# Performance work log

Hardware: AMD Instinct MI355X
Metric: run time of the kernel (lower is better)

The kernel has to match this reference:

```python
import jax, jax.numpy as jnp
import numpy as np

HIDDEN = 1024
HEADS = 16
HEAD = HIDDEN // HEADS  # 64, rotary_emb_dim == head dim
B = 8
S = 1024  # max_seqlen; all sequences full length
WINDOW = (64, 64)  # sliding_window=128 -> (64, 64)
ROPE_BASE = 10000.0


def _rope_cos_sin(seqlen, dim, base):
    inv_freq = 1.0 / (base ** (jnp.arange(0, dim, 2, dtype=jnp.float32) / dim))
    t = jnp.arange(seqlen, dtype=jnp.float32)
    freqs = jnp.outer(t, inv_freq)  # [S, dim/2]
    return jnp.cos(freqs), jnp.sin(freqs)


def _apply_rope(x, cos, sin):
    # x: [B, S, H, D], non-interleaved rotary over full head dim
    d2 = cos.shape[-1]
    x1, x2 = x[..., :d2], x[..., d2:]
    c = cos[None, :, None, :]
    s = sin[None, :, None, :]
    return jnp.concatenate([x1 * c - x2 * s, x2 * c + x1 * s], axis=-1)


def setup_inputs() -> dict:
    key = jax.random.key(0)
    k1, k2, k3 = jax.random.split(key, 3)
    hidden_states = jax.random.normal(k1, (B * S, HIDDEN), dtype=jnp.float32)
    cu_seqlens = jnp.arange(B + 1, dtype=jnp.int32) * S
    indices = jnp.arange(B * S, dtype=jnp.int32)
    attn_mask = jnp.ones((B, S), dtype=jnp.int32)
    Wqkv = jax.random.normal(k2, (3 * HIDDEN, HIDDEN), dtype=jnp.float32) * 0.02
    Wo = jax.random.normal(k3, (HIDDEN, HIDDEN), dtype=jnp.float32) * 0.02
    return {
        'hidden_states': hidden_states,
        'cu_seqlens': cu_seqlens,
        'max_seqlen': S,
        'indices': indices,
        'attn_mask': attn_mask,
        'Wqkv': Wqkv,
        'Wo': Wo,
    }


def reference(hidden_states, cu_seqlens, max_seqlen, indices, attn_mask, Wqkv, Wo):
    # QKV projection on unpadded tokens: [T, 3*H*D]
    qkv = hidden_states @ Wqkv.T
    qkv = qkv.reshape(B, S, 3, HEADS, HEAD)
    # Rotary positions reset per sequence; all sequences are full length S.
    cos, sin = _rope_cos_sin(S, HEAD, ROPE_BASE)
    q = _apply_rope(qkv[:, :, 0], cos, sin)
    k = _apply_rope(qkv[:, :, 1], cos, sin)
    v = qkv[:, :, 2]
    scores = jnp.einsum('bshd,bthd->bhst', q, k) / jnp.sqrt(jnp.float32(HEAD))
    # sliding-window mask: key j visible to query i iff i-left <= j <= i+right
    i = jnp.arange(S)[:, None]
    j = jnp.arange(S)[None, :]
    win = (j >= i - WINDOW[0]) & (j <= i + WINDOW[1])  # [S, S]
    key_mask = attn_mask.astype(bool)[:, None, None, :]  # [B,1,1,S]
    mask = win[None, None, :, :] & key_mask
    scores = jnp.where(mask, scores, jnp.finfo(scores.dtype).min)
    probs = jax.nn.softmax(scores, axis=-1)
    attn = jnp.einsum('bhst,bthd->bshd', probs, v).reshape(B * S, HIDDEN)
    return attn @ Wo.T
```

## Files before the change

### kernel.cpp

```cpp
#include <hip/hip_runtime.h>


typedef __attribute__((ext_vector_type(8))) short short8;
typedef __attribute__((ext_vector_type(4))) float f32x4;

#define SEQ   1024
#define NHEAD 16
#define HEADD 64
#define NTOK  8192

__device__ __forceinline__ unsigned short f2bf(float x) {
  unsigned u = __float_as_uint(x);
  u += 0x7fffu + ((u >> 16) & 1u);
  return (unsigned short)(u >> 16);
}

__device__ __forceinline__ void gload_lds16(const void* g, void* l) {
  __builtin_amdgcn_global_load_lds((__attribute__((address_space(1))) void*)(g),
                                   (__attribute__((address_space(3))) void*)(l),
                                   16, 0, 0);
}

__global__ __launch_bounds__(256) void prep(
    const float* __restrict__ hidden, const float* __restrict__ Wqkv,
    const float* __restrict__ Wo,
    unsigned short* __restrict__ hb, unsigned short* __restrict__ wqb,
    unsigned short* __restrict__ wob, float2* __restrict__ tab) {
  int bid = blockIdx.x;
  const float* in; unsigned short* out; int i;
  if (bid < 8192)       { in = hidden; out = hb;  i = bid * 256 + threadIdx.x; }
  else if (bid < 11264) { in = Wqkv;   out = wqb; i = (bid - 8192) * 256 + threadIdx.x; }
  else if (bid < 12288) { in = Wo;     out = wob; i = (bid - 11264) * 256 + threadIdx.x; }
  else {
    int j = (bid - 12288) * 256 + threadIdx.x;
    int s = j >> 5, d = j & 31;
    float inv = exp2f(-(float)d * 0.41524101186092034f);
    float sn, cs;
    sincosf((float)s * inv, &sn, &cs);
    tab[j] = make_float2(cs, sn);
    return;
  }
  float4 v = ((const float4*)in)[i];
  ushort4 o;
  o.x = f2bf(v.x); o.y = f2bf(v.y); o.z = f2bf(v.z); o.w = f2bf(v.w);
  ((ushort4*)out)[i] = o;
}

__global__ __launch_bounds__(256) void gemm_qkv_rope(
    const unsigned short* __restrict__ A,
    const unsigned short* __restrict__ W,
    const float2* __restrict__ tab,
    unsigned short* __restrict__ qb,
    unsigned short* __restrict__ kb,
    unsigned short* __restrict__ vt)
{
  __shared__ unsigned short As[128 * 32];
  __shared__ unsigned short Bs[128 * 32];
  const int tid  = threadIdx.x;
  const int wave = tid >> 6, lane = tid & 63;
  const int quad = lane >> 4, l15 = lane & 15;
  const int bid  = blockIdx.x;
  const int xcd  = bid & 7, idx = bid >> 3;
  const int rb   = xcd * 8 + (idx & 7);
  const int cb   = idx >> 3;
  const int row0 = rb * 128;
  const int col0 = cb * 128;
  const int mrow = (wave >> 1) * 64;
  const int ncol = (wave & 1) * 64;
  const int qs8  = (quad ^ ((l15 >> 1) & 3)) * 8;

  f32x4 acc[4][4];
#pragma unroll
  for (int i = 0; i < 4; i++)
#pragma unroll
    for (int j = 0; j < 4; j++) acc[i][j] = (f32x4){0.f, 0.f, 0.f, 0.f};

  for (int k0 = 0; k0 < 1024; k0 += 32) {
#pragma unroll
    for (int i = 0; i < 2; i++) {
      int p = i * 256 + tid;
      int r = p >> 2, c = p & 3;
      int cs = c ^ ((r >> 1) & 3);
      gload_lds16(A + (size_t)(row0 + r) * 1024 + k0 + cs * 8, &As[p * 8]);
      gload_lds16(W + (size_t)(col0 + r) * 1024 + k0 + cs * 8, &Bs[p * 8]);
    }
    __syncthreads();
    short8 af[4], bf[4];
#pragma unroll
    for (int mt = 0; mt < 4; mt++)
      af[mt] = *(const short8*)&As[(mrow + mt * 16 + l15) * 32 + qs8];
#pragma unroll
    for (int nt = 0; nt < 4; nt++)
      bf[nt] = *(const short8*)&Bs[(ncol + nt * 16 + l15) * 32 + qs8];
#pragma unroll
    for (int mt = 0; mt < 4; mt++)
#pragma unroll
      for (int nt = 0; nt < 4; nt++)
        acc[mt][nt] = __builtin_amdgcn_mfma_f32_16x16x32_bf16(af[mt], bf[nt],
                                                              acc[mt][nt], 0, 0, 0);
    __syncthreads();
  }

  const int colw  = col0 + ncol;
  const int which = colw >> 10;
  const int h     = (colw >> 6) & 15;
  const int rowg  = row0 + mrow;

  if (which == 2) {
#pragma unroll
    for (int mt = 0; mt < 4; mt++) {
      int rbase = rowg + mt * 16 + quad * 4;
      int b = rbase >> 10, s = rbase & 1023;
#pragma unroll
      for (int c = 0; c < 4; c++) {
        int d = c * 16 + l15;
        ushort4 o;
        o.x = f2bf(acc[mt][c][0]); o.y = f2bf(acc[mt][c][1]);
        o.z = f2bf(acc[mt][c][2]); o.w = f2bf(acc[mt][c][3]);
        *(ushort4*)&vt[((size_t)((b * 16 + h) * 64 + d)) * 1024 + s] = o;
      }
    }
  } else {
    unsigned short* dst = (which == 0) ? qb : kb;
    const float scale = (which == 0) ? 0.125f : 1.0f;
#pragma unroll
    for (int mt = 0; mt < 4; mt++) {
#pragma unroll
      for (int r = 0; r < 4; r++) {
        int row = rowg + mt * 16 + quad * 4 + r;
        int b = row >> 10, s = row & 1023;
        size_t base = (size_t)((b * 16 + h) * 1024 + s) * 64;
        float2 t0 = tab[s * 32 + l15];
        float2 t1 = tab[s * 32 + 16 + l15];
        float x1a = acc[mt][0][r], x2a = acc[mt][2][r];
        float x1b = acc[mt][1][r], x2b = acc[mt][3][r];
        dst[base + l15]           = f2bf((x1a * t0.x - x2a * t0.y) * scale);
        dst[base + 32 + l15]      = f2bf((x2a * t0.x + x1a * t0.y) * scale);
        dst[base + 16 + l15]      = f2bf((x1b * t1.x - x2b * t1.y) * scale);
        dst[base + 48 + l15]      = f2bf((x2b * t1.x + x1b * t1.y) * scale);
      }
    }
  }
}

__global__ __launch_bounds__(256) void attn_win(
    const unsigned short* __restrict__ qb,
    const unsigned short* __restrict__ kb,
    const unsigned short* __restrict__ vt,
    const int* __restrict__ am,
    unsigned short* __restrict__ ob)
{
  __shared__ unsigned short Ks[192 * 68];
  __shared__ unsigned short Vs[64 * 196];
  __shared__ unsigned short smask[192];

  const int tid  = threadIdx.x;
  const int wave = tid >> 6, lane = tid & 63;
  const int quad = lane >> 4, l15 = lane & 15;
  const int b  = blockIdx.x >> 4, h = blockIdx.x & 15;
  const int qs = blockIdx.y * 64;
  const size_t hb = (size_t)(b * 16 + h);
  const unsigned short* Qg = qb + hb * SEQ * 64;
  const unsigned short* Kg = kb + hb * SEQ * 64;
  const unsigned short* Vg = vt + hb * 64 * SEQ;
  const int t0 = qs - 64;

#pragma unroll
  for (int i = 0; i < 6; i++) {
    int p = i * 256 + tid;
    int r = p >> 3, c = p & 7;
    int t = t0 + r; t = t < 0 ? 0 : (t > 1023 ? 1023 : t);
    *(short8*)&Ks[r * 68 + c * 8] = *(const short8*)&Kg[(size_t)t * 64 + c * 8];
  }
#pragma unroll
  for (int i = 0; i < 6; i++) {
    int p = i * 256 + tid;
    int d = p / 24, c = p % 24;
    int t = t0 + c * 8; t = t < 0 ? 0 : (t > 1016 ? 1016 : t);
    *(short8*)&Vs[d * 196 + c * 8] = *(const short8*)&Vg[(size_t)d * SEQ + t];
  }
  if (tid < 192) {
    int t = t0 + tid;
    smask[tid] = (t >= 0 && t < SEQ) ? (unsigned short)(am[b * SEQ + t] != 0) : 0;
  }
  __syncthreads();

  const int qw = qs + wave * 16;
  short8 qf0 = *(const short8*)&Qg[(size_t)(qw + l15) * 64 + quad * 8];
  short8 qf1 = *(const short8*)&Qg[(size_t)(qw + l15) * 64 + 32 + quad * 8];

  f32x4 sc[12];
#pragma unroll
  for (int tt = 0; tt < 12; tt++) {
    short8 b0 = *(const short8*)&Ks[(tt * 16 + l15) * 68 + quad * 8];
    short8 b1 = *(const short8*)&Ks[(tt * 16 + l15) * 68 + 32 + quad * 8];
    f32x4 a = (f32x4){0.f, 0.f, 0.f, 0.f};
    a = __builtin_amdgcn_mfma_f32_16x16x32_bf16(qf0, b0, a, 0, 0, 0);
    a = __builtin_amdgcn_mfma_f32_16x16x32_bf16(qf1, b1, a, 0, 0, 0);
    sc[tt] = a;
  }

  float lrow[4];
#pragma unroll
  for (int r = 0; r < 4; r++) {
    int i = qw + quad * 4 + r;
    float mx = -3e38f;
#pragma unroll
    for (int tt = 0; tt < 12; tt++) {
      int t = t0 + tt * 16 + l15;
      bool ok = (t >= i - 64) && (t <= i + 64) && smask[tt * 16 + l15];
      float v = ok ? sc[tt][r] : -3e38f;
      sc[tt][r] = v;
      mx = fmaxf(mx, v);
    }
#pragma unroll
    for (int off = 1; off < 16; off <<= 1) mx = fmaxf(mx, __shfl_xor(mx, off));
    float sum = 0.f;
#pragma unroll
    for (int tt = 0; tt < 12; tt++) {
      float p = __expf(sc[tt][r] - mx);
      sc[tt][r] = p;
      sum += p;
    }
#pragma unroll
    for (int off = 1; off < 16; off <<= 1) sum += __shfl_xor(sum, off);
    lrow[r] = sum;
  }

  __syncthreads();
  unsigned short* Pw = &Ks[wave * (16 * 196)];
#pragma unroll
  for (int tt = 0; tt < 12; tt++)
#pragma unroll
    for (int r = 0; r < 4; r++)
      Pw[(quad * 4 + r) * 196 + tt * 16 + l15] = f2bf(sc[tt][r]);
  __syncthreads();

  f32x4 o[4];
#pragma unroll
  for (int dt = 0; dt < 4; dt++) o[dt] = (f32x4){0.f, 0.f, 0.f, 0.f};
#pragma unroll
  for (int kt = 0; kt < 6; kt++) {
    short8 pf = *(const short8*)&Pw[l15 * 196 + kt * 32 + quad * 8];
#pragma unroll
    for (int dt = 0; dt < 4; dt++) {
      short8 vf = *(const short8*)&Vs[(dt * 16 + l15) * 196 + kt * 32 + quad * 8];
      o[dt] = __builtin_amdgcn_mfma_f32_16x16x32_bf16(pf, vf, o[dt], 0, 0, 0);
    }
  }

#pragma unroll
  for (int r = 0; r < 4; r++) {
    float inv = 1.f / lrow[r];
    int tok = b * SEQ + qw + quad * 4 + r;
    size_t base = (size_t)tok * 1024 + h * 64;
#pragma unroll
    for (int dt = 0; dt < 4; dt++)
      ob[base + dt * 16 + l15] = f2bf(o[dt][r] * inv);
  }
}

__global__ __launch_bounds__(256) void gemm_out(
    const unsigned short* __restrict__ A,
    const unsigned short* __restrict__ W,
    float* __restrict__ out)
{
  __shared__ unsigned short As[128 * 32];
  __shared__ unsigned short Bs[128 * 32];
  const int tid  = threadIdx.x;
  const int wave = tid >> 6, lane = tid & 63;
  const int quad = lane >> 4, l15 = lane & 15;
  const int bid  = blockIdx.x;
  const int xcd  = bid & 7, idx = bid >> 3;
  const int row0 = (xcd * 8 + (idx & 7)) * 128;
  const int col0 = (idx >> 3) * 128;
  const int mrow = (wave >> 1) * 64;
  const int ncol = (wave & 1) * 64;
  const int qs8  = (quad ^ ((l15 >> 1) & 3)) * 8;

  f32x4 acc[4][4];
#pragma unroll
  for (int i = 0; i < 4; i++)
#pragma unroll
    for (int j = 0; j < 4; j++) acc[i][j] = (f32x4){0.f, 0.f, 0.f, 0.f};

  for (int k0 = 0; k0 < 1024; k0 += 32) {
#pragma unroll
    for (int i = 0; i < 2; i++) {
      int p = i * 256 + tid;
      int r = p >> 2, c = p & 3;
      int cs = c ^ ((r >> 1) & 3);
      gload_lds16(A + (size_t)(row0 + r) * 1024 + k0 + cs * 8, &As[p * 8]);
      gload_lds16(W + (size_t)(col0 + r) * 1024 + k0 + cs * 8, &Bs[p * 8]);
    }
    __syncthreads();
    short8 af[4], bf[4];
#pragma unroll
    for (int mt = 0; mt < 4; mt++)
      af[mt] = *(const short8*)&As[(mrow + mt * 16 + l15) * 32 + qs8];
#pragma unroll
    for (int nt = 0; nt < 4; nt++)
      bf[nt] = *(const short8*)&Bs[(ncol + nt * 16 + l15) * 32 + qs8];
#pragma unroll
    for (int mt = 0; mt < 4; mt++)
#pragma unroll
      for (int nt = 0; nt < 4; nt++)
        acc[mt][nt] = __builtin_amdgcn_mfma_f32_16x16x32_bf16(af[mt], bf[nt],
                                                              acc[mt][nt], 0, 0, 0);
    __syncthreads();
  }

  const int colw = col0 + ncol;
  const int rowg = row0 + mrow;
#pragma unroll
  for (int mt = 0; mt < 4; mt++)
#pragma unroll
    for (int r = 0; r < 4; r++) {
      int row = rowg + mt * 16 + quad * 4 + r;
#pragma unroll
      for (int nt = 0; nt < 4; nt++)
        out[(size_t)row * 1024 + colw + nt * 16 + l15] = acc[mt][nt][r];
    }
}

extern "C" void kernel_launch(void* const* d_in, const int* in_sizes, int n_in,
                              void* d_out, int out_size, void* d_ws, size_t ws_size,
                              hipStream_t stream) {
  const float* hidden = (const float*)d_in[0];
  const int*   am     = (const int*)d_in[4];
  const float* Wqkv   = (const float*)d_in[5];
  const float* Wo     = (const float*)d_in[6];
  float* out = (float*)d_out;

  char* ws = (char*)d_ws;
  unsigned short* hb  = (unsigned short*)(ws);
  unsigned short* wqb = (unsigned short*)(ws + (size_t)(16 << 20));
  unsigned short* wob = (unsigned short*)(ws + (size_t)(22 << 20));
  unsigned short* qbf = (unsigned short*)(ws + (size_t)(24 << 20));
  unsigned short* kbf = (unsigned short*)(ws + (size_t)(40 << 20));
  unsigned short* vtb = (unsigned short*)(ws + (size_t)(56 << 20));
  float2*         tab = (float2*)(ws + (size_t)(72 << 20));
  unsigned short* ab  = hb;

  prep<<<12416, 256, 0, stream>>>(hidden, Wqkv, Wo, hb, wqb, wob, tab);

  gemm_qkv_rope<<<1536, 256, 0, stream>>>(hb, wqb, tab, qbf, kbf, vtb);

  dim3 g2(128, 16);
  attn_win<<<g2, 256, 0, stream>>>(qbf, kbf, vtb, am, ab);

  gemm_out<<<512, 256, 0, stream>>>(ab, wob, out);
}
```

Baseline: 234.2 us.

## Fuse windowed attention and output GEMM into persistent kernel with grid barrier

New measurement: 311.9 us. 33.2% more time.

```diff
diff --git a/kernel.cpp b/kernel.cpp
--- a/kernel.cpp
+++ b/kernel.cpp
@@ -8,6 +8,7 @@
 #define NHEAD 16
 #define HEADD 64
 #define NTOK  8192
+#define FBLK  512
 
 __device__ __forceinline__ unsigned short f2bf(float x) {
   unsigned u = __float_as_uint(x);
@@ -19,6 +20,10 @@
   __builtin_amdgcn_global_load_lds((__attribute__((address_space(1))) void*)(g),
                                    (__attribute__((address_space(3))) void*)(l),
                                    16, 0, 0);
+}
+
+__global__ void binit(unsigned* bar) {
+  if (threadIdx.x < 2) bar[threadIdx.x] = 0u;
 }
 
 __global__ __launch_bounds__(256) void prep(
@@ -143,184 +148,201 @@
   }
 }
 
-__global__ __launch_bounds__(256) void attn_win(
+__global__ __launch_bounds__(256, 2) void attn_gemm2(
     const unsigned short* __restrict__ qb,
     const unsigned short* __restrict__ kb,
     const unsigned short* __restrict__ vt,
     const int* __restrict__ am,
-    unsigned short* __restrict__ ob)
+    unsigned short* __restrict__ ab,
+    const unsigned short* __restrict__ W,
+    float* __restrict__ out,
+    unsigned* __restrict__ bar)
 {
-  __shared__ unsigned short Ks[192 * 68];
-  __shared__ unsigned short Vs[64 * 196];
-  __shared__ unsigned short smask[192];
+  __shared__ union {
+    struct { unsigned short Ks[192 * 68];
+             unsigned short Vs[64 * 196];
+             unsigned short smask[192]; } a;
+    struct { unsigned short As[128 * 32];
+             unsigned short Bs[128 * 32]; } g;
+  } sm;
 
   const int tid  = threadIdx.x;
   const int wave = tid >> 6, lane = tid & 63;
   const int quad = lane >> 4, l15 = lane & 15;
-  const int b  = blockIdx.x >> 4, h = blockIdx.x & 15;
-  const int qs = blockIdx.y * 64;
+  const int bid  = blockIdx.x;
+
+  const int x = bid & 127;
+  const int b = x >> 4, h = x & 15;
   const size_t hb = (size_t)(b * 16 + h);
   const unsigned short* Qg = qb + hb * SEQ * 64;
   const unsigned short* Kg = kb + hb * SEQ * 64;
   const unsigned short* Vg = vt + hb * 64 * SEQ;
-  const int t0 = qs - 64;
-
-#pragma unroll
-  for (int i = 0; i < 6; i++) {
-    int p = i * 256 + tid;
-    int r = p >> 3, c = p & 7;
-    int t = t0 + r; t = t < 0 ? 0 : (t > 1023 ? 1023 : t);
-    *(short8*)&Ks[r * 68 + c * 8] = *(const short8*)&Kg[(size_t)t * 64 + c * 8];
-  }
-#pragma unroll
-  for (int i = 0; i < 6; i++) {
-    int p = i * 256 + tid;
-    int d = p / 24, c = p % 24;
-    int t = t0 + c * 8; t = t < 0 ? 0 : (t > 1016 ? 1016 : t);
-    *(short8*)&Vs[d * 196 + c * 8] = *(const short8*)&Vg[(size_t)d * SEQ + t];
-  }
-  if (tid < 192) {
-    int t = t0 + tid;
-    smask[tid] = (t >= 0 && t < SEQ) ? (unsigned short)(am[b * SEQ + t] != 0) : 0;
-  }
+
+  for (int it = 0; it < 4; it++) {
+    const int qt = ((bid >> 7) + 4 * it) & 15;
+    const int qs = qt * 64;
+    const int t0 = qs - 64;
+    __syncthreads();
+
+#pragma unroll
+    for (int i = 0; i < 6; i++) {
+      int p = i * 256 + tid;
+      int r = p >> 3, c = p & 7;
+      int t = t0 + r; t = t < 0 ? 0 : (t > 1023 ? 1023 : t);
+      *(short8*)&sm.a.Ks[r * 68 + c * 8] =
+          *(const short8*)&Kg[(size_t)t * 64 + c * 8];
+    }
+#pragma unroll
+    for (int i = 0; i < 6; i++) {
+      int p = i * 256 + tid;
+      int d = p / 24, c = p % 24;
+      int t = t0 + c * 8; t = t < 0 ? 0 : (t > 1016 ? 1016 : t);
+      *(short8*)&sm.a.Vs[d * 196 + c * 8] =
+          *(const short8*)&Vg[(size_t)d * SEQ + t];
+    }
+    if (tid < 192) {
+      int t = t0 + tid;
+      sm.a.smask[tid] = (t >= 0 && t < SEQ)
+                          ? (unsigned short)(am[b * SEQ + t] != 0) : 0;
+    }
+    __syncthreads();
+
+    const int qw = qs + wave * 16;
+    short8 qf0 = *(const short8*)&Qg[(size_t)(qw + l15) * 64 + quad * 8];
+    short8 qf1 = *(const short8*)&Qg[(size_t)(qw + l15) * 64 + 32 + quad * 8];
+
+    f32x4 sc[12];
+#pragma unroll
+    for (int tt = 0; tt < 12; tt++) {
+      short8 b0 = *(const short8*)&sm.a.Ks[(tt * 16 + l15) * 68 + quad * 8];
+      short8 b1 = *(const short8*)&sm.a.Ks[(tt * 16 + l15) * 68 + 32 + quad * 8];
+      f32x4 a = (f32x4){0.f, 0.f, 0.f, 0.f};
+      a = __builtin_amdgcn_mfma_f32_16x16x32_bf16(qf0, b0, a, 0, 0, 0);
+      a = __builtin_amdgcn_mfma_f32_16x16x32_bf16(qf1, b1, a, 0, 0, 0);
+      sc[tt] = a;
+    }
+
+    float lrow[4];
+#pragma unroll
+    for (int r = 0; r < 4; r++) {
+      int i = qw + quad * 4 + r;
+      float sum = 0.f;
+#pragma unroll
+      for (int tt = 0; tt < 12; tt++) {
+        int t = t0 + tt * 16 + l15;
+        bool ok = (t >= i - 64) && (t <= i + 64) && sm.a.smask[tt * 16 + l15];
+        float p = ok ? __expf(sc[tt][r]) : 0.f;
+        sc[tt][r] = p;
+        sum += p;
+      }
+#pragma unroll
+      for (int off = 1; off < 16; off <<= 1) sum += __shfl_xor(sum, off);
+      lrow[r] = sum;
+    }
+
+    __syncthreads();
+    unsigned short* Pw = &sm.a.Ks[wave * (16 * 196)];
+#pragma unroll
+    for (int tt = 0; tt < 12; tt++)
+#pragma unroll
+      for (int r = 0; r < 4; r++)
+        Pw[(quad * 4 + r) * 196 + tt * 16 + l15] = f2bf(sc[tt][r]);
+    __syncthreads();
+
+    f32x4 o[4];
+#pragma unroll
+    for (int dt = 0; dt < 4; dt++) o[dt] = (f32x4){0.f, 0.f, 0.f, 0.f};
+#pragma unroll
+    for (int kt = 0; kt < 6; kt++) {
+      short8 pf = *(const short8*)&Pw[l15 * 196 + kt * 32 + quad * 8];
+#pragma unroll
+      for (int dt = 0; dt < 4; dt++) {
+        short8 vf = *(const short8*)&sm.a.Vs[(dt * 16 + l15) * 196 +
+                                             kt * 32 + quad * 8];
+        o[dt] = __builtin_amdgcn_mfma_f32_16x16x32_bf16(pf, vf, o[dt], 0, 0, 0);
+      }
+    }
+
+#pragma unroll
+    for (int r = 0; r < 4; r++) {
+      float inv = 1.f / lrow[r];
+      int tok = b * SEQ + qw + quad * 4 + r;
+      size_t base = (size_t)tok * 1024 + h * 64;
+#pragma unroll
+      for (int dt = 0; dt < 4; dt++)
+        ab[base + dt * 16 + l15] = f2bf(o[dt][r] * inv);
+    }
+  }
+
   __syncthreads();
-
-  const int qw = qs + wave * 16;
-  short8 qf0 = *(const short8*)&Qg[(size_t)(qw + l15) * 64 + quad * 8];
-  short8 qf1 = *(const short8*)&Qg[(size_t)(qw + l15) * 64 + 32 + quad * 8];
-
-  f32x4 sc[12];
-#pragma unroll
-  for (int tt = 0; tt < 12; tt++) {
-    short8 b0 = *(const short8*)&Ks[(tt * 16 + l15) * 68 + quad * 8];
-    short8 b1 = *(const short8*)&Ks[(tt * 16 + l15) * 68 + 32 + quad * 8];
-    f32x4 a = (f32x4){0.f, 0.f, 0.f, 0.f};
-    a = __builtin_amdgcn_mfma_f32_16x16x32_bf16(qf0, b0, a, 0, 0, 0);
-    a = __builtin_amdgcn_mfma_f32_16x16x32_bf16(qf1, b1, a, 0, 0, 0);
-    sc[tt] = a;
-  }
-
-  float lrow[4];
-#pragma unroll
-  for (int r = 0; r < 4; r++) {
-    int i = qw + quad * 4 + r;
-    float mx = -3e38f;
-#pragma unroll
-    for (int tt = 0; tt < 12; tt++) {
-      int t = t0 + tt * 16 + l15;
-      bool ok = (t >= i - 64) && (t <= i + 64) && smask[tt * 16 + l15];
-      float v = ok ? sc[tt][r] : -3e38f;
-      sc[tt][r] = v;
-      mx = fmaxf(mx, v);
-    }
-#pragma unroll
-    for (int off = 1; off < 16; off <<= 1) mx = fmaxf(mx, __shfl_xor(mx, off));
-    float sum = 0.f;
-#pragma unroll
-    for (int tt = 0; tt < 12; tt++) {
-      float p = __expf(sc[tt][r] - mx);
-      sc[tt][r] = p;
-      sum += p;
-    }
-#pragma unroll
-    for (int off = 1; off < 16; off <<= 1) sum += __shfl_xor(sum, off);
-    lrow[r] = sum;
-  }
-
+  if (tid == 0) {
+    __threadfence();
+    unsigned a = atomicAdd(&bar[0], 1u);
+    if (a == (unsigned)gridDim.x - 1u) {
+      __threadfence();
+      atomicExch(&bar[1], 1u);
+    } else {
+      for (unsigned sp = 0; sp < (1u << 21); sp++) {
+        if (atomicAdd(&bar[1], 0u) != 0u) break;
+        __builtin_amdgcn_s_sleep(8);
+      }
+    }
+    __threadfence();
+  }
   __syncthreads();
-  unsigned short* Pw = &Ks[wave * (16 * 196)];
-#pragma unroll
-  for (int tt = 0; tt < 12; tt++)
-#pragma unroll
-    for (int r = 0; r < 4; r++)
-      Pw[(quad * 4 + r) * 196 + tt * 16 + l15] = f2bf(sc[tt][r]);
-  __syncthreads();
-
-  f32x4 o[4];
-#pragma unroll
-  for (int dt = 0; dt < 4; dt++) o[dt] = (f32x4){0.f, 0.f, 0.f, 0.f};
-#pragma unroll
-  for (int kt = 0; kt < 6; kt++) {
-    short8 pf = *(const short8*)&Pw[l15 * 196 + kt * 32 + quad * 8];
-#pragma unroll
-    for (int dt = 0; dt < 4; dt++) {
-      short8 vf = *(const short8*)&Vs[(dt * 16 + l15) * 196 + kt * 32 + quad * 8];
-      o[dt] = __builtin_amdgcn_mfma_f32_16x16x32_bf16(pf, vf, o[dt], 0, 0, 0);
-    }
-  }
-
-#pragma unroll
-  for (int r = 0; r < 4; r++) {
-    float inv = 1.f / lrow[r];
-    int tok = b * SEQ + qw + quad * 4 + r;
-    size_t base = (size_t)tok * 1024 + h * 64;
-#pragma unroll
-    for (int dt = 0; dt < 4; dt++)
-      ob[base + dt * 16 + l15] = f2bf(o[dt][r] * inv);
-  }
-}
-
-__global__ __launch_bounds__(256) void gemm_out(
-    const unsigned short* __restrict__ A,
-    const unsigned short* __restrict__ W,
-    float* __restrict__ out)
-{
-  __shared__ unsigned short As[128 * 32];
-  __shared__ unsigned short Bs[128 * 32];
-  const int tid  = threadIdx.x;
-  const int wave = tid >> 6, lane = tid & 63;
-  const int quad = lane >> 4, l15 = lane & 15;
-  const int bid  = blockIdx.x;
-  const int xcd  = bid & 7, idx = bid >> 3;
-  const int row0 = (xcd * 8 + (idx & 7)) * 128;
-  const int col0 = (idx >> 3) * 128;
-  const int mrow = (wave >> 1) * 64;
-  const int ncol = (wave & 1) * 64;
-  const int qs8  = (quad ^ ((l15 >> 1) & 3)) * 8;
-
-  f32x4 acc[4][4];
-#pragma unroll
-  for (int i = 0; i < 4; i++)
-#pragma unroll
-    for (int j = 0; j < 4; j++) acc[i][j] = (f32x4){0.f, 0.f, 0.f, 0.f};
-
-  for (int k0 = 0; k0 < 1024; k0 += 32) {
-#pragma unroll
-    for (int i = 0; i < 2; i++) {
-      int p = i * 256 + tid;
-      int r = p >> 2, c = p & 3;
-      int cs = c ^ ((r >> 1) & 3);
-      gload_lds16(A + (size_t)(row0 + r) * 1024 + k0 + cs * 8, &As[p * 8]);
-      gload_lds16(W + (size_t)(col0 + r) * 1024 + k0 + cs * 8, &Bs[p * 8]);
-    }
-    __syncthreads();
-    short8 af[4], bf[4];
+
+  {
+    const int xcd  = bid & 7, idx = bid >> 3;
+    const int row0 = (xcd * 8 + (idx & 7)) * 128;
+    const int col0 = (idx >> 3) * 128;
+    const int mrow = (wave >> 1) * 64;
+    const int ncol = (wave & 1) * 64;
+    const int qs8  = (quad ^ ((l15 >> 1) & 3)) * 8;
+
+    f32x4 acc[4][4];
+#pragma unroll
+    for (int i = 0; i < 4; i++)
+#pragma unroll
+      for (int j = 0; j < 4; j++) acc[i][j] = (f32x4){0.f, 0.f, 0.f, 0.f};
+
+    for (int k0 = 0; k0 < 1024; k0 += 32) {
+#pragma unroll
+      for (int i = 0; i < 2; i++) {
+        int p = i * 256 + tid;
+        int r = p >> 2, c = p & 3;
+        int cs = c ^ ((r >> 1) & 3);
+        gload_lds16(ab + (size_t)(row0 + r) * 1024 + k0 + cs * 8, &sm.g.As[p * 8]);
+        gload_lds16(W + (size_t)(col0 + r) * 1024 + k0 + cs * 8, &sm.g.Bs[p * 8]);
+      }
+      __syncthreads();
+      short8 af[4], bf[4];
+#pragma unroll
+      for (int mt = 0; mt < 4; mt++)
+        af[mt] = *(const short8*)&sm.g.As[(mrow + mt * 16 + l15) * 32 + qs8];
+#pragma unroll
+      for (int nt = 0; nt < 4; nt++)
+        bf[nt] = *(const short8*)&sm.g.Bs[(ncol + nt * 16 + l15) * 32 + qs8];
+#pragma unroll
+      for (int mt = 0; mt < 4; mt++)
+#pragma unroll
+        for (int nt = 0; nt < 4; nt++)
+          acc[mt][nt] = __builtin_amdgcn_mfma_f32_16x16x32_bf16(af[mt], bf[nt],
+                                                                acc[mt][nt], 0, 0, 0);
+      __syncthreads();
+    }
+
+    const int colw = col0 + ncol;
+    const int rowg = row0 + mrow;
 #pragma unroll
     for (int mt = 0; mt < 4; mt++)
-      af[mt] = *(const short8*)&As[(mrow + mt * 16 + l15) * 32 + qs8];
-#pragma unroll
-    for (int nt = 0; nt < 4; nt++)
-      bf[nt] = *(const short8*)&Bs[(ncol + nt * 16 + l15) * 32 + qs8];
-#pragma unroll
-    for (int mt = 0; mt < 4; mt++)
-#pragma unroll
-      for (int nt = 0; nt < 4; nt++)
-        acc[mt][nt] = __builtin_amdgcn_mfma_f32_16x16x32_bf16(af[mt], bf[nt],
-                                                              acc[mt][nt], 0, 0, 0);
-    __syncthreads();
-  }
-
-  const int colw = col0 + ncol;
-  const int rowg = row0 + mrow;
-#pragma unroll
-  for (int mt = 0; mt < 4; mt++)
-#pragma unroll
-    for (int r = 0; r < 4; r++) {
-      int row = rowg + mt * 16 + quad * 4 + r;
-#pragma unroll
-      for (int nt = 0; nt < 4; nt++)
-        out[(size_t)row * 1024 + colw + nt * 16 + l15] = acc[mt][nt][r];
-    }
+#pragma unroll
+      for (int r = 0; r < 4; r++) {
+        int row = rowg + mt * 16 + quad * 4 + r;
+#pragma unroll
+        for (int nt = 0; nt < 4; nt++)
+          out[(size_t)row * 1024 + colw + nt * 16 + l15] = acc[mt][nt][r];
+      }
+  }
 }
 
 extern "C" void kernel_launch(void* const* d_in, const int* in_sizes, int n_in,
@@ -340,14 +362,14 @@
   unsigned short* kbf = (unsigned short*)(ws + (size_t)(40 << 20));
   unsigned short* vtb = (unsigned short*)(ws + (size_t)(56 << 20));
   float2*         tab = (float2*)(ws + (size_t)(72 << 20));
+  unsigned*       bar = (unsigned*)(ws + (size_t)(73 << 20));
   unsigned short* ab  = hb;
 
+  binit<<<1, 64, 0, stream>>>(bar);
+
   prep<<<12416, 256, 0, stream>>>(hidden, Wqkv, Wo, hb, wqb, wob, tab);
 
   gemm_qkv_rope<<<1536, 256, 0, stream>>>(hb, wqb, tab, qbf, kbf, vtb);
 
-  dim3 g2(128, 16);
-  attn_win<<<g2, 256, 0, stream>>>(qbf, kbf, vtb, am, ab);
-
-  gemm_out<<<512, 256, 0, stream>>>(ab, wob, out);
-}
+  attn_gemm2<<<FBLK, 256, 0, stream>>>(qbf, kbf, vtb, am, ab, wob, out, bar);
+}
```
